# Kernel optimization log

Hardware: AMD Instinct MI355X
Metric: run time of the kernel (lower is better)

Reference implementation:

```python
import jax, jax.numpy as jnp
import numpy as np

B, N, M, H = 4, 1024, 1024, 64
IK, IQ, IV, IT = 3, 3, 5, 1


def _mlp(x, W1, b1, W2, b2):
    # Linear -> ReLU -> Linear  (matches torch.nn.Sequential in the module)
    return jax.nn.relu(x @ W1 + b1) @ W2 + b2


def setup_inputs() -> dict:
    key = jax.random.key(0)
    ks = jax.random.split(key, 18)
    rn = lambda k, s, sc: (jax.random.normal(k, s, jnp.float32) * sc)
    inp = {
        "coords_f": rn(ks[0], (B, N, IK), 1.0),
        "values_f": rn(ks[1], (B, N, IV), 1.0),
        "coords_t": rn(ks[2], (B, M, IQ), 1.0),
        # Wk MLP
        "Wk1": rn(ks[3], (IK, H), 1.0 / np.sqrt(IK)), "bk1": jnp.zeros((H,), jnp.float32),
        "Wk2": rn(ks[4], (H, H), 1.0 / np.sqrt(H)),   "bk2": jnp.zeros((H,), jnp.float32),
        # Wq MLP
        "Wq1": rn(ks[5], (IQ, H), 1.0 / np.sqrt(IQ)), "bq1": jnp.zeros((H,), jnp.float32),
        "Wq2": rn(ks[6], (H, H), 1.0 / np.sqrt(H)),   "bq2": jnp.zeros((H,), jnp.float32),
        # Wv MLP
        "Wv1": rn(ks[7], (IV, H), 1.0 / np.sqrt(IV)), "bv1": jnp.zeros((H,), jnp.float32),
        "Wv2": rn(ks[8], (H, H), 1.0 / np.sqrt(H)),   "bv2": jnp.zeros((H,), jnp.float32),
        # Output projection
        "Wo": rn(ks[9], (H, IT), 1.0 / np.sqrt(H)),   "bo": jnp.zeros((IT,), jnp.float32),
    }
    return inp


def reference(coords_f, values_f, coords_t,
              Wk1, bk1, Wk2, bk2,
              Wq1, bq1, Wq2, bq2,
              Wv1, bv1, Wv2, bv2,
              Wo, bo):
    K = _mlp(coords_f, Wk1, bk1, Wk2, bk2)   # [B, N, H]
    Q = _mlp(coords_t, Wq1, bq1, Wq2, bq2)   # [B, M, H]
    V = _mlp(values_f, Wv1, bv1, Wv2, bv2)   # [B, N, H]
    # L1 cdist: score[b, n, m] = sum_h |K[b,n,h] - Q[b,m,h]|
    score = jnp.abs(K[:, :, None, :] - Q[:, None, :, :]).sum(-1)  # [B, N, M]
    # custom NW kernel: softmax over keys (axis=1) of -d^2/2
    att = jax.nn.softmax(-0.5 * score * score, axis=1)            # [B, N, M]
    out = jnp.einsum('bnm,bnh->bmh', att, V)                      # [B, M, H]
    return out @ Wo + bo                                          # [B, M, IT]
```

## Files before the change

kernel.cpp:

```cpp
#include <hip/hip_runtime.h>
#include <math.h>

#define BB 4
#define NN 1024
#define MM 1024
#define HH 64
#define NT 8
#define BN 128
#define BM 64
#define MT (MM / BM)

static constexpr float NEG_BIG = -3.0e38f;
static constexpr float SCALE = -0.72134752044448170f;

__global__ __launch_bounds__(256)
void prep_kernel(const float* __restrict__ coords_f,
                 const float* __restrict__ values_f,
                 const float* __restrict__ coords_t,
                 const float* __restrict__ Wk1, const float* __restrict__ bk1,
                 const float* __restrict__ Wk2, const float* __restrict__ bk2,
                 const float* __restrict__ Wq1, const float* __restrict__ bq1,
                 const float* __restrict__ Wq2, const float* __restrict__ bq2,
                 const float* __restrict__ Wv1, const float* __restrict__ bv1,
                 const float* __restrict__ Wv2, const float* __restrict__ bv2,
                 const float* __restrict__ Wo,
                 float* __restrict__ Kout, float* __restrict__ Qout,
                 float* __restrict__ vhat) {
    const int bx = blockIdx.x;
    const int tid = threadIdx.x;

    if (bx < 256) {
        const int type = bx >> 7;
        const int sub = bx & 127;
        const int row = (sub >> 3) * 256 + tid;
        const int co  = (sub & 7) * 8;

        const float* in = type ? coords_t : coords_f;
        const float* W1 = type ? Wq1 : Wk1;
        const float* b1 = type ? bq1 : bk1;
        const float* W2 = type ? Wq2 : Wk2;
        const float* b2 = type ? bq2 : bk2;
        float* out = type ? Qout : Kout;

        const float in0 = in[row * 3 + 0];
        const float in1 = in[row * 3 + 1];
        const float in2 = in[row * 3 + 2];

        float acc[8];
#pragma unroll
        for (int j = 0; j < 8; ++j) acc[j] = b2[co + j];

        for (int hi = 0; hi < HH; ++hi) {
            float h = b1[hi];
            h = fmaf(in0, W1[hi], h);
            h = fmaf(in1, W1[64 + hi], h);
            h = fmaf(in2, W1[128 + hi], h);
            h = fmaxf(h, 0.0f);
            const float* w = W2 + hi * 64 + co;
#pragma unroll
            for (int j = 0; j < 8; ++j) acc[j] = fmaf(h, w[j], acc[j]);
        }
#pragma unroll
        for (int j = 0; j < 8; ++j) out[row * 64 + co + j] = acc[j];
    } else {
        const int sub = bx - 256;
        __shared__ float w2o[64];
        __shared__ float b2o_sh;
        if (tid < 64) {
            float s = 0.0f;
            for (int ho = 0; ho < 64; ++ho) s = fmaf(Wv2[tid * 64 + ho], Wo[ho], s);
            w2o[tid] = s;
        }
        if (tid == 0) {
            float s = 0.0f;
            for (int ho = 0; ho < 64; ++ho) s = fmaf(bv2[ho], Wo[ho], s);
            b2o_sh = s;
        }
        __syncthreads();

        const int row = sub * 256 + tid;
        const float* vin = values_f + row * 5;
        const float i0 = vin[0], i1 = vin[1], i2 = vin[2], i3 = vin[3], i4 = vin[4];

        float s = b2o_sh;
        for (int j = 0; j < HH; ++j) {
            float h = bv1[j];
            h = fmaf(i0, Wv1[j], h);
            h = fmaf(i1, Wv1[64 + j], h);
            h = fmaf(i2, Wv1[128 + j], h);
            h = fmaf(i3, Wv1[192 + j], h);
            h = fmaf(i4, Wv1[256 + j], h);
            h = fmaxf(h, 0.0f);
            s = fmaf(h, w2o[j], s);
        }
        vhat[row] = s;
    }
}

__global__ __launch_bounds__(256, 2)
void fused_kernel(const float* __restrict__ Kb,
                  const float* __restrict__ Qb,
                  const float* __restrict__ vh,
                  float* __restrict__ mxp,
                  float* __restrict__ denp,
                  float* __restrict__ nump) {
    __shared__ float kt[BN * 64];
    __shared__ float qt[BM * 64];

    const int tid = threadIdx.x;
    const int nt = blockIdx.x, mt = blockIdx.y, b = blockIdx.z;
    const int n0 = nt * BN, m0 = mt * BM;
    const int ty = tid >> 4, tx = tid & 15;

    float4* kt4 = reinterpret_cast<float4*>(kt);
    float4* qt4 = reinterpret_cast<float4*>(qt);

    {
        const float4* ksrc = reinterpret_cast<const float4*>(Kb + (b * NN + n0) * 64);
#pragma unroll
        for (int l = 0; l < 8; ++l) {
            const int fidx = l * 256 + tid;
            const int row = fidx >> 4, h4 = fidx & 15;
            kt4[row * 16 + (h4 ^ (row & 7))] = ksrc[fidx];
        }
        const float4* qsrc = reinterpret_cast<const float4*>(Qb + (b * MM + m0) * 64);
#pragma unroll
        for (int l = 0; l < 4; ++l) {
            const int fidx = l * 256 + tid;
            const int row = fidx >> 4, h4 = fidx & 15;
            qt4[row * 16 + (h4 ^ (row & 7))] = qsrc[fidx];
        }
    }
    __syncthreads();

    const int swk = ty & 7;
    const int swq = tx & 7;

    const float4* kbase = kt4 + ty * 16;
    const float4* qbase = qt4 + tx * 16;

    float acc[8][4];
#pragma unroll
    for (int i = 0; i < 8; ++i)
#pragma unroll
        for (int j = 0; j < 4; ++j) acc[i][j] = 0.0f;

#pragma unroll
    for (int h4 = 0; h4 < 16; ++h4) {
        float4 kv[8], qv[4];
        const int ck = h4 ^ swk;
        const int cq = h4 ^ swq;
#pragma unroll
        for (int ni = 0; ni < 8; ++ni)
            kv[ni] = kbase[ni * 256 + ck];
#pragma unroll
        for (int mj = 0; mj < 4; ++mj)
            qv[mj] = qbase[mj * 256 + cq];
#pragma unroll
        for (int ni = 0; ni < 8; ++ni)
#pragma unroll
            for (int mj = 0; mj < 4; ++mj) {
                acc[ni][mj] += fabsf(kv[ni].x - qv[mj].x);
                acc[ni][mj] += fabsf(kv[ni].y - qv[mj].y);
                acc[ni][mj] += fabsf(kv[ni].z - qv[mj].z);
                acc[ni][mj] += fabsf(kv[ni].w - qv[mj].w);
            }
    }

    float vloc[8];
#pragma unroll
    for (int ni = 0; ni < 8; ++ni) vloc[ni] = vh[b * NN + n0 + ni * 16 + ty];

    float mxr[4], denr[4], numr[4];
#pragma unroll
    for (int mj = 0; mj < 4; ++mj) {
        float a[8];
#pragma unroll
        for (int ni = 0; ni < 8; ++ni) {
            const float d = acc[ni][mj];
            a[ni] = d * d * SCALE;
        }
        const float mx = fmaxf(fmaxf(fmaxf(a[0], a[1]), fmaxf(a[2], a[3])),
                               fmaxf(fmaxf(a[4], a[5]), fmaxf(a[6], a[7])));
        float den = 0.0f, num = 0.0f;
#pragma unroll
        for (int ni = 0; ni < 8; ++ni) {
            const float p = __builtin_amdgcn_exp2f(a[ni] - mx);
            den += p;
            num = fmaf(p, vloc[ni], num);
        }
        mxr[mj] = mx; denr[mj] = den; numr[mj] = num;
    }

    __syncthreads();
    float* red = kt;
#pragma unroll
    for (int mj = 0; mj < 4; ++mj) {
        const int base = (ty * 64 + mj * 16 + tx) * 3;
        red[base + 0] = mxr[mj];
        red[base + 1] = denr[mj];
        red[base + 2] = numr[mj];
    }
    __syncthreads();

    if (tid < 64) {
        float M = NEG_BIG, D = 0.0f, Nu = 0.0f;
        for (int t = 0; t < 16; ++t) {
            const int base = (t * 64 + tid) * 3;
            const float m2 = red[base + 0];
            const float d2 = red[base + 1];
            const float n2 = red[base + 2];
            const float nm = fmaxf(M, m2);
            const float s0 = __builtin_amdgcn_exp2f(M - nm);
            const float s1 = __builtin_amdgcn_exp2f(m2 - nm);
            D  = D * s0 + d2 * s1;
            Nu = Nu * s0 + n2 * s1;
            M = nm;
        }
        const int p = nt * (BB * MM) + b * MM + m0 + tid;
        mxp[p] = M; denp[p] = D; nump[p] = Nu;
    }
}

__global__ __launch_bounds__(64)
void combine_kernel(const float* __restrict__ mxp,
                    const float* __restrict__ denp,
                    const float* __restrict__ nump,
                    const float* __restrict__ bo,
                    float* __restrict__ out) {
    const int bm = blockIdx.x * 64 + threadIdx.x;
    float M = NEG_BIG, D = 0.0f, Nu = 0.0f;
#pragma unroll
    for (int nt = 0; nt < NT; ++nt) {
        const int idx = nt * (BB * MM) + bm;
        const float m2 = mxp[idx];
        const float d2 = denp[idx];
        const float n2 = nump[idx];
        const float nm = fmaxf(M, m2);
        const float s0 = __builtin_amdgcn_exp2f(M - nm);
        const float s1 = __builtin_amdgcn_exp2f(m2 - nm);
        D  = D * s0 + d2 * s1;
        Nu = Nu * s0 + n2 * s1;
        M = nm;
    }
    out[bm] = Nu / D + bo[0];
}

extern "C" void kernel_launch(void* const* d_in, const int* in_sizes, int n_in,
                              void* d_out, int out_size, void* d_ws, size_t ws_size,
                              hipStream_t stream) {
    const float* coords_f = (const float*)d_in[0];
    const float* values_f = (const float*)d_in[1];
    const float* coords_t = (const float*)d_in[2];
    const float* Wk1 = (const float*)d_in[3];
    const float* bk1 = (const float*)d_in[4];
    const float* Wk2 = (const float*)d_in[5];
    const float* bk2 = (const float*)d_in[6];
    const float* Wq1 = (const float*)d_in[7];
    const float* bq1 = (const float*)d_in[8];
    const float* Wq2 = (const float*)d_in[9];
    const float* bq2 = (const float*)d_in[10];
    const float* Wv1 = (const float*)d_in[11];
    const float* bv1 = (const float*)d_in[12];
    const float* Wv2 = (const float*)d_in[13];
    const float* bv2 = (const float*)d_in[14];
    const float* Wo  = (const float*)d_in[15];
    const float* bo  = (const float*)d_in[16];

    float* ws  = (float*)d_ws;
    float* Kb  = ws;
    float* Qb  = Kb + BB * NN * HH;
    float* vh  = Qb + BB * MM * HH;
    float* mxp = vh + BB * NN;
    float* denp = mxp + NT * BB * MM;
    float* nump = denp + NT * BB * MM;

    prep_kernel<<<dim3(272), 256, 0, stream>>>(
        coords_f, values_f, coords_t,
        Wk1, bk1, Wk2, bk2, Wq1, bq1, Wq2, bq2,
        Wv1, bv1, Wv2, bv2, Wo, Kb, Qb, vh);

    fused_kernel<<<dim3(NT, MT, BB), 256, 0, stream>>>(
        Kb, Qb, vh, mxp, denp, nump);

    combine_kernel<<<dim3(64), 64, 0, stream>>>(
        mxp, denp, nump, bo, (float*)d_out);
}
```

Measured before the change: 27.14 us.

## Use direct global-to-LDS loads, split prep work finer, and flatten combine

The fused kernel now stages K and Q tiles with global_load_lds, applying the XOR swizzle on the global source address. This skips the register round trip, and the vh loads move ahead of the barrier so they overlap with it. The reduction buffer gets its own shared array, which removes one barrier but adds about 12KB of LDS and may lower occupancy. The prep kernel doubles its block count with 4 output columns per thread and vector stores, and combine takes a single max then sums with one exp2 per tile.

```diff
diff --git a/kernel.cpp b/kernel.cpp
--- a/kernel.cpp
+++ b/kernel.cpp
@@ -12,6 +12,13 @@
 
 static constexpr float NEG_BIG = -3.0e38f;
 static constexpr float SCALE = -0.72134752044448170f;
+
+__device__ __forceinline__ void gload16(const void* gsrc, void* lds_base) {
+    __builtin_amdgcn_global_load_lds(
+        (const __attribute__((address_space(1))) void*)gsrc,
+        (__attribute__((address_space(3))) void*)lds_base,
+        16, 0, 0);
+}
 
 __global__ __launch_bounds__(256)
 void prep_kernel(const float* __restrict__ coords_f,
@@ -29,11 +36,11 @@
     const int bx = blockIdx.x;
     const int tid = threadIdx.x;
 
-    if (bx < 256) {
-        const int type = bx >> 7;
-        const int sub = bx & 127;
-        const int row = (sub >> 3) * 256 + tid;
-        const int co  = (sub & 7) * 8;
+    if (bx < 512) {
+        const int type = bx >> 8;
+        const int sub = bx & 255;
+        const int row = (sub >> 4) * 256 + tid;
+        const int co  = (sub & 15) * 4;
 
         const float* in = type ? coords_t : coords_f;
         const float* W1 = type ? Wq1 : Wk1;
@@ -46,10 +53,11 @@
         const float in1 = in[row * 3 + 1];
         const float in2 = in[row * 3 + 2];
 
-        float acc[8];
-#pragma unroll
-        for (int j = 0; j < 8; ++j) acc[j] = b2[co + j];
-
+        float acc[4];
+#pragma unroll
+        for (int j = 0; j < 4; ++j) acc[j] = b2[co + j];
+
+#pragma unroll 4
         for (int hi = 0; hi < HH; ++hi) {
             float h = b1[hi];
             h = fmaf(in0, W1[hi], h);
@@ -58,12 +66,12 @@
             h = fmaxf(h, 0.0f);
             const float* w = W2 + hi * 64 + co;
 #pragma unroll
-            for (int j = 0; j < 8; ++j) acc[j] = fmaf(h, w[j], acc[j]);
-        }
-#pragma unroll
-        for (int j = 0; j < 8; ++j) out[row * 64 + co + j] = acc[j];
+            for (int j = 0; j < 4; ++j) acc[j] = fmaf(h, w[j], acc[j]);
+        }
+        float4* o = reinterpret_cast<float4*>(out + row * 64 + co);
+        *o = make_float4(acc[0], acc[1], acc[2], acc[3]);
     } else {
-        const int sub = bx - 256;
+        const int sub = bx - 512;
         __shared__ float w2o[64];
         __shared__ float b2o_sh;
         if (tid < 64) {
@@ -106,36 +114,40 @@
                   float* __restrict__ nump) {
     __shared__ float kt[BN * 64];
     __shared__ float qt[BM * 64];
+    __shared__ float red[16 * 64 * 3];
 
     const int tid = threadIdx.x;
     const int nt = blockIdx.x, mt = blockIdx.y, b = blockIdx.z;
     const int n0 = nt * BN, m0 = mt * BM;
     const int ty = tid >> 4, tx = tid & 15;
-
-    float4* kt4 = reinterpret_cast<float4*>(kt);
-    float4* qt4 = reinterpret_cast<float4*>(qt);
-
-    {
-        const float4* ksrc = reinterpret_cast<const float4*>(Kb + (b * NN + n0) * 64);
-#pragma unroll
-        for (int l = 0; l < 8; ++l) {
-            const int fidx = l * 256 + tid;
-            const int row = fidx >> 4, h4 = fidx & 15;
-            kt4[row * 16 + (h4 ^ (row & 7))] = ksrc[fidx];
-        }
-        const float4* qsrc = reinterpret_cast<const float4*>(Qb + (b * MM + m0) * 64);
-#pragma unroll
-        for (int l = 0; l < 4; ++l) {
-            const int fidx = l * 256 + tid;
-            const int row = fidx >> 4, h4 = fidx & 15;
-            qt4[row * 16 + (h4 ^ (row & 7))] = qsrc[fidx];
-        }
-    }
+    const int wv = tid >> 6;
+
+    const float4* ksrc = reinterpret_cast<const float4*>(Kb + (b * NN + n0) * 64);
+    const float4* qsrc = reinterpret_cast<const float4*>(Qb + (b * MM + m0) * 64);
+
+#pragma unroll
+    for (int l = 0; l < 8; ++l) {
+        const int fidx = l * 256 + tid;
+        const int row = fidx >> 4, col = fidx & 15;
+        gload16(ksrc + row * 16 + (col ^ (row & 7)), kt + (l * 256 + wv * 64) * 4);
+    }
+#pragma unroll
+    for (int l = 0; l < 4; ++l) {
+        const int fidx = l * 256 + tid;
+        const int row = fidx >> 4, col = fidx & 15;
+        gload16(qsrc + row * 16 + (col ^ (row & 7)), qt + (l * 256 + wv * 64) * 4);
+    }
+
+    float vloc[8];
+#pragma unroll
+    for (int ni = 0; ni < 8; ++ni) vloc[ni] = vh[b * NN + n0 + ni * 16 + ty];
+
     __syncthreads();
 
+    const float4* kt4 = reinterpret_cast<const float4*>(kt);
+    const float4* qt4 = reinterpret_cast<const float4*>(qt);
     const int swk = ty & 7;
     const int swq = tx & 7;
-
     const float4* kbase = kt4 + ty * 16;
     const float4* qbase = qt4 + tx * 16;
 
@@ -167,10 +179,6 @@
             }
     }
 
-    float vloc[8];
-#pragma unroll
-    for (int ni = 0; ni < 8; ++ni) vloc[ni] = vh[b * NN + n0 + ni * 16 + ty];
-
     float mxr[4], denr[4], numr[4];
 #pragma unroll
     for (int mj = 0; mj < 4; ++mj) {
@@ -192,8 +200,6 @@
         mxr[mj] = mx; denr[mj] = den; numr[mj] = num;
     }
 
-    __syncthreads();
-    float* red = kt;
 #pragma unroll
     for (int mj = 0; mj < 4; ++mj) {
         const int base = (ty * 64 + mj * 16 + tx) * 3;
@@ -229,19 +235,22 @@
                     const float* __restrict__ bo,
                     float* __restrict__ out) {
     const int bm = blockIdx.x * 64 + threadIdx.x;
-    float M = NEG_BIG, D = 0.0f, Nu = 0.0f;
-#pragma unroll
-    for (int nt = 0; nt < NT; ++nt) {
-        const int idx = nt * (BB * MM) + bm;
-        const float m2 = mxp[idx];
-        const float d2 = denp[idx];
-        const float n2 = nump[idx];
-        const float nm = fmaxf(M, m2);
-        const float s0 = __builtin_amdgcn_exp2f(M - nm);
-        const float s1 = __builtin_amdgcn_exp2f(m2 - nm);
-        D  = D * s0 + d2 * s1;
-        Nu = Nu * s0 + n2 * s1;
-        M = nm;
+    float m[NT], d[NT], n[NT];
+#pragma unroll
+    for (int t = 0; t < NT; ++t) {
+        const int idx = t * (BB * MM) + bm;
+        m[t] = mxp[idx];
+        d[t] = denp[idx];
+        n[t] = nump[idx];
+    }
+    const float M = fmaxf(fmaxf(fmaxf(m[0], m[1]), fmaxf(m[2], m[3])),
+                          fmaxf(fmaxf(m[4], m[5]), fmaxf(m[6], m[7])));
+    float D = 0.0f, Nu = 0.0f;
+#pragma unroll
+    for (int t = 0; t < NT; ++t) {
+        const float s = __builtin_amdgcn_exp2f(m[t] - M);
+        D  = fmaf(d[t], s, D);
+        Nu = fmaf(n[t], s, Nu);
     }
     out[bm] = Nu / D + bo[0];
 }
@@ -275,7 +284,7 @@
     float* denp = mxp + NT * BB * MM;
     float* nump = denp + NT * BB * MM;
 
-    prep_kernel<<<dim3(272), 256, 0, stream>>>(
+    prep_kernel<<<dim3(528), 256, 0, stream>>>(
         coords_f, values_f, coords_t,
         Wk1, bk1, Wk2, bk2, Wq1, bq1, Wq2, bq2,
         Wv1, bv1, Wv2, bv2, Wo, Kb, Qb, vh);
```

Result: slower. 27.81 us (+2.5%).
